# Kernel optimization log

Measured on AMD Instinct MI355X. Metric: run time of the kernel, lower is better.

The kernel has to match this reference:

```python
import jax, jax.numpy as jnp
import numpy as np

FEAT = 128
SCALE = FEAT ** -0.5

def _linear(x, W, b):
    # torch nn.Linear: y = x @ W.T + b, W: [out, in]
    return jnp.einsum('bnd,od->bno', x, W) + b

def setup_inputs() -> dict:
    key = jax.random.key(0)
    ks = jax.random.split(key, 12)
    B, N1, N2 = 2, 4096, 32768
    inp = {
        'sparse_xyz':  jax.random.normal(ks[0], (B, N1, 3),    dtype=jnp.float32),
        'sparse_feat': jax.random.normal(ks[1], (B, N1, FEAT), dtype=jnp.float32),
        'dense_xyz':   jax.random.normal(ks[2], (B, N2, 3),    dtype=jnp.float32),
        'dense_feat':  jax.random.normal(ks[3], (B, N2, FEAT), dtype=jnp.float32),
    }
    s_in = (FEAT + 3) ** -0.5  # torch Linear default init bound ~ 1/sqrt(in)
    s_f = FEAT ** -0.5
    inp['Wq'] = jax.random.uniform(ks[4], (FEAT, FEAT + 3), jnp.float32, -s_in, s_in)
    inp['bq'] = jax.random.uniform(ks[5], (FEAT,), jnp.float32, -s_in, s_in)
    inp['Wk'] = jax.random.uniform(ks[6], (FEAT, FEAT + 3), jnp.float32, -s_in, s_in)
    inp['bk'] = jax.random.uniform(ks[7], (FEAT,), jnp.float32, -s_in, s_in)
    inp['Wv'] = jax.random.uniform(ks[8], (FEAT, FEAT), jnp.float32, -s_f, s_f)
    inp['bv'] = jax.random.uniform(ks[9], (FEAT,), jnp.float32, -s_f, s_f)
    inp['Wo'] = jax.random.uniform(ks[10], (FEAT, FEAT), jnp.float32, -s_f, s_f)
    inp['bo'] = jax.random.uniform(ks[11], (FEAT,), jnp.float32, -s_f, s_f)
    return inp

def reference(sparse_xyz, sparse_feat, dense_xyz, dense_feat,
              Wq, bq, Wk, bk, Wv, bv, Wo, bo):
    # Projections
    Q = _linear(jnp.concatenate([dense_xyz, dense_feat], axis=-1), Wq, bq)   # [B,N2,F]
    K = _linear(jnp.concatenate([sparse_xyz, sparse_feat], axis=-1), Wk, bk) # [B,N1,F]
    V = _linear(sparse_feat, Wv, bv)                                          # [B,N1,F]
    # Attention scores with euclidean distance penalty (torch.cdist, p=2)
    scores = jnp.einsum('bqf,bkf->bqk', Q, K) * SCALE                         # [B,N2,N1]
    sq = (jnp.sum(dense_xyz**2, -1)[:, :, None]
          + jnp.sum(sparse_xyz**2, -1)[:, None, :]
          - 2.0 * jnp.einsum('bqd,bkd->bqk', dense_xyz, sparse_xyz))
    dist = jnp.sqrt(jnp.maximum(sq, 1e-12))
    attn = jax.nn.softmax(scores - 0.5 * dist, axis=-1)                       # [B,N2,N1]
    propagated = jnp.einsum('bqk,bkf->bqf', attn, V)                          # [B,N2,F]
    return _linear(propagated + dense_feat, Wo, bo)
```

## Files before the change

kernel.cpp:

```cpp
#include <hip/hip_runtime.h>
#include <stdint.h>

#define NB 2
#define N1 4096
#define N2 32768
#define DD 128
#define KT 32
#define NTILES (N1 / KT)
static constexpr float SCLE = 0.1275174306f;
static constexpr float CNEG = -0.7213475204444817f;
static constexpr float THR  = 11.5415603f;

typedef float f32x16 __attribute__((ext_vector_type(16)));
typedef __bf16 bf16x8v __attribute__((ext_vector_type(8)));
typedef __bf16 bf16x2v __attribute__((ext_vector_type(2)));
typedef unsigned int u32;
typedef unsigned short u16;

union FragU { uint4 u; bf16x8v b; };

__device__ __forceinline__ u16 f2bf(float f) {
  __bf16 h = (__bf16)f;
  return __builtin_bit_cast(u16, h);
}
__device__ __forceinline__ u32 pk2(float lo, float hi) {
  bf16x2v v; v[0] = (__bf16)lo; v[1] = (__bf16)hi;
  return __builtin_bit_cast(u32, v);
}
__device__ __forceinline__ float bfhi(float f) { return (float)(__bf16)f; }
__device__ __forceinline__ float m3(float a, float b, float c) {
  return fmaxf(fmaxf(a, b), c);
}
__device__ __forceinline__ f32x16 MFMA(uint4 a, uint4 b, const f32x16& c) {
  FragU A, B; A.u = a; B.u = b;
  return __builtin_amdgcn_mfma_f32_32x32x16_bf16(A.b, B.b, c, 0, 0, 0);
}
__device__ __forceinline__ uint4 packhi8(float4 a, float4 b) {
  return make_uint4(pk2(a.x, a.y), pk2(a.z, a.w), pk2(b.x, b.y), pk2(b.z, b.w));
}
__device__ __forceinline__ uint4 packlo8(float4 a, float4 b) {
  return make_uint4(pk2(a.x - bfhi(a.x), a.y - bfhi(a.y)),
                    pk2(a.z - bfhi(a.z), a.w - bfhi(a.w)),
                    pk2(b.x - bfhi(b.x), b.y - bfhi(b.y)),
                    pk2(b.z - bfhi(b.z), b.w - bfhi(b.w)));
}
__device__ __forceinline__ uint4 conv8(float a0, float a1, float a2, float a3,
                                       float a4, float a5, float a6, float a7, int h) {
  u32 A0 = pk2(a0, a1), A1 = pk2(a2, a3);
  u32 B0 = pk2(a4, a5), B1 = pk2(a6, a7);
  u32 A0s = (u32)__shfl_xor((int)A0, 32);
  u32 A1s = (u32)__shfl_xor((int)A1, 32);
  u32 B0s = (u32)__shfl_xor((int)B0, 32);
  u32 B1s = (u32)__shfl_xor((int)B1, 32);
  return h ? make_uint4(B0s, B1s, B0, B1) : make_uint4(A0, A1, A0s, A1s);
}

__global__ __launch_bounds__(256) void prep_kv(
    const float* __restrict__ sxyz, const float* __restrict__ sfeat,
    const float* __restrict__ Wk, const float* __restrict__ bk,
    const float* __restrict__ Wv, const float* __restrict__ bv,
    u16* __restrict__ Kws, u16* __restrict__ VTws, u16* __restrict__ EKws) {
  const int tid = threadIdx.x;
  const int l = tid & 63, w = tid >> 6, h = l >> 5, ln = l & 31;
  const int b = blockIdx.x >> 7;
  const int kb = (blockIdx.x & 127) * 32;
  const int key = kb + ln;
  const size_t frow = (size_t)(b * N1 + key) * DD;

  uint4 xf[8];
#pragma unroll
  for (int s = 0; s < 8; ++s) {
    const float4* fp = (const float4*)(sfeat + frow + s * 16 + h * 8);
    xf[s] = packhi8(fp[0], fp[1]);
  }
  const float* xp = sxyz + (size_t)(b * N1 + key) * 3;
  float sx = xp[0], sy = xp[1], sz = xp[2];
  uint4 x8 = h ? make_uint4(0, 0, 0, 0)
               : make_uint4(pk2(sx, sy), pk2(sz, 0.f), 0u, 0u);

  f32x16 kacc, vacc;
#pragma unroll
  for (int r = 0; r < 16; ++r) {
    int o = (r & 3) + 8 * (r >> 2) + 4 * h + 32 * w;
    kacc[r] = bk[o];
    vacc[r] = bv[o];
  }

  const int outd = ln + 32 * w;
  const float* wkr = Wk + (size_t)outd * 131;
  const float* wvr = Wv + (size_t)outd * DD;
#pragma unroll
  for (int s = 0; s < 8; ++s) {
    const float* p = wkr + 3 + s * 16 + h * 8;
    uint4 wa = make_uint4(pk2(p[0], p[1]), pk2(p[2], p[3]),
                          pk2(p[4], p[5]), pk2(p[6], p[7]));
    kacc = MFMA(wa, xf[s], kacc);
    const float4* q = (const float4*)(wvr + s * 16 + h * 8);
    vacc = MFMA(packhi8(q[0], q[1]), xf[s], vacc);
  }
  {
    uint4 w8 = h ? make_uint4(0, 0, 0, 0)
                 : make_uint4(pk2(wkr[0], wkr[1]), pk2(wkr[2], 0.f), 0u, 0u);
    kacc = MFMA(w8, x8, kacc);
  }

#pragma unroll
  for (int rq = 0; rq < 4; ++rq) {
    uint2 kv;
    kv.x = pk2(kacc[rq * 4 + 0], kacc[rq * 4 + 1]);
    kv.y = pk2(kacc[rq * 4 + 2], kacc[rq * 4 + 3]);
    *(uint2*)&Kws[(size_t)(b * N1 + key) * DD + w * 32 + rq * 8 + h * 4] = kv;
  }
#pragma unroll
  for (int r = 0; r < 16; ++r) {
    int o = (r & 3) + 8 * (r >> 2) + 4 * h + 32 * w;
    VTws[(size_t)(b * DD + o) * N1 + key] = f2bf(vacc[r]);
  }

  if (tid < 32) {
    int k2i = kb + tid;
    const float* xq = sxyz + (size_t)(b * N1 + k2i) * 3;
    float x = xq[0], y = xq[1], z = xq[2];
    float k2 = x * x + y * y + z * z;
    float xh = bfhi(x), xl = x - xh;
    float yh = bfhi(y), yl = y - yh;
    float zh = bfhi(z), zl = z - zh;
    float k2h = bfhi(k2), k2l = k2 - k2h;
    uint4 e0 = make_uint4(pk2(xh, xl), pk2(xh, yh), pk2(yl, yh), pk2(zh, zl));
    uint4 e1 = make_uint4(pk2(zh, k2h), pk2(k2l, 1.f), pk2(1.f, 0.f), 0u);
    uint4* dst = (uint4*)&EKws[(size_t)(b * N1 + k2i) * 16];
    dst[0] = e0;
    dst[1] = e1;
  }
}

__global__ __launch_bounds__(256, 1) void attn_fwd(
    const float* __restrict__ dxyz, const float* __restrict__ dfeat,
    const float* __restrict__ Wq, const float* __restrict__ bq,
    const float* __restrict__ Wo, const float* __restrict__ bo,
    const u16* __restrict__ Kws, const u16* __restrict__ VTws,
    const u16* __restrict__ EKws, float* __restrict__ out) {
  __shared__ __align__(16) u16 sm[8192];

  const int tid = threadIdx.x;
  const int l = tid & 63, w = tid >> 6, h = l >> 5, ln = l & 31;
  const int b = blockIdx.x >> 7;
  const int qb = (blockIdx.x & 127) * 256;
  const int bN1 = b * N1;
  size_t qrow[2];
  qrow[0] = (size_t)(b * N2 + qb + w * 64 + ln);
  qrow[1] = qrow[0] + 32;

  f32x16 zf;
#pragma unroll
  for (int r = 0; r < 16; ++r) zf[r] = 0.f;

  uint4 eq[2];
  float qx[2], qy[2], qz[2];
#pragma unroll
  for (int g = 0; g < 2; ++g) {
    const float* xp = dxyz + qrow[g] * 3;
    float x = xp[0], y = xp[1], z = xp[2];
    float q2 = x * x + y * y + z * z;
    float xh = bfhi(x), xl = x - xh, yh = bfhi(y), yl = y - yh, zh = bfhi(z), zl = z - zh;
    float q2h = bfhi(q2), q2l = q2 - q2h;
    eq[g] = h ? make_uint4(pk2(-2.f * zl, 1.f), pk2(1.f, q2h), pk2(q2l, 0.f), 0u)
              : make_uint4(pk2(-2.f * xh, -2.f * xh), pk2(-2.f * xl, -2.f * yh),
                           pk2(-2.f * yh, -2.f * yl), pk2(-2.f * zh, -2.f * zh));
    qx[g] = x; qy[g] = y; qz[g] = z;
  }

  uint4 qf[2][8];
  {
    uint4 xf[2][8], x8[2];
#pragma unroll
    for (int g = 0; g < 2; ++g) {
#pragma unroll
      for (int s = 0; s < 8; ++s) {
        const float4* fp = (const float4*)(dfeat + qrow[g] * DD + s * 16 + h * 8);
        xf[g][s] = packhi8(fp[0], fp[1]);
      }
      x8[g] = h ? make_uint4(0, 0, 0, 0)
                : make_uint4(pk2(qx[g], qy[g]), pk2(qz[g], 0.f), 0u, 0u);
    }
#pragma unroll
    for (int ot = 0; ot < 4; ++ot) {
      f32x16 qt[2];
#pragma unroll
      for (int r = 0; r < 16; ++r) {
        float bqv = SCLE * bq[(r & 3) + 8 * (r >> 2) + 4 * h + 32 * ot];
        qt[0][r] = bqv; qt[1][r] = bqv;
      }
      const float* wqr = Wq + (size_t)(ln + 32 * ot) * 131;
#pragma unroll
      for (int s = 0; s < 8; ++s) {
        const float* p = wqr + 3 + s * 16 + h * 8;
        uint4 wa = make_uint4(pk2(SCLE * p[0], SCLE * p[1]), pk2(SCLE * p[2], SCLE * p[3]),
                              pk2(SCLE * p[4], SCLE * p[5]), pk2(SCLE * p[6], SCLE * p[7]));
        qt[0] = MFMA(wa, xf[0][s], qt[0]);
        qt[1] = MFMA(wa, xf[1][s], qt[1]);
      }
      uint4 w8 = h ? make_uint4(0, 0, 0, 0)
                   : make_uint4(pk2(SCLE * wqr[0], SCLE * wqr[1]), pk2(SCLE * wqr[2], 0.f), 0u, 0u);
      qt[0] = MFMA(w8, x8[0], qt[0]);
      qt[1] = MFMA(w8, x8[1], qt[1]);
#pragma unroll
      for (int g = 0; g < 2; ++g) {
        qf[g][2 * ot] = conv8(qt[g][0], qt[g][1], qt[g][2], qt[g][3],
                              qt[g][4], qt[g][5], qt[g][6], qt[g][7], h);
        qf[g][2 * ot + 1] = conv8(qt[g][8], qt[g][9], qt[g][10], qt[g][11],
                                  qt[g][12], qt[g][13], qt[g][14], qt[g][15], h);
      }
    }
  }

  f32x16 oacc[2][4];
#pragma unroll
  for (int g = 0; g < 2; ++g)
#pragma unroll
    for (int ft = 0; ft < 4; ++ft)
#pragma unroll
      for (int r = 0; r < 16; ++r) oacc[g][ft][r] = 0.f;
  float m[2] = {-1e30f, -1e30f}, lsum[2] = {0.f, 0.f};

  const int kr = tid >> 4, kd = tid & 15;
  const int vr = tid >> 2, vd = tid & 3;
  const int kswz = (kd ^ (kr & 7)) * 8;
  const int vswz = (vd ^ ((vr >> 1) & 3)) * 8;
  const int vx = (ln >> 1) & 3;
  const u16* Kb = Kws + (size_t)bN1 * DD;
  const u16* Vb = VTws + (size_t)b * DD * N1;
  uint4 k0g, k1g, v0g, v1g;

#define LOADT(kt)                                                            \
  do {                                                                       \
    k0g = *(const uint4*)&Kb[(size_t)((kt) + kr) * DD + kd * 8];             \
    k1g = *(const uint4*)&Kb[(size_t)((kt) + kr + 16) * DD + kd * 8];        \
    v0g = *(const uint4*)&Vb[(size_t)vr * N1 + (kt) + vd * 8];               \
    v1g = *(const uint4*)&Vb[(size_t)(vr + 64) * N1 + (kt) + vd * 8];        \
  } while (0)
#define WRITET()                                                             \
  do {                                                                       \
    *(uint4*)&sm[kr * 128 + kswz] = k0g;                                     \
    *(uint4*)&sm[(kr + 16) * 128 + kswz] = k1g;                              \
    *(uint4*)&sm[4096 + vr * 32 + vswz] = v0g;                               \
    *(uint4*)&sm[4096 + (vr + 64) * 32 + vswz] = v1g;                        \
  } while (0)

  LOADT(0);
  WRITET();
  uint4 ek = *(const uint4*)&EKws[(size_t)(bN1 + ln) * 16 + h * 8];

  for (int t = 0; t < NTILES; ++t) {
    __syncthreads();
    const bool more = (t + 1 < NTILES);
    if (more) LOADT((t + 1) * KT);

    f32x16 sacc[2];
    sacc[0] = MFMA(ek, eq[0], zf);
    sacc[1] = MFMA(ek, eq[1], zf);
#pragma unroll
    for (int g = 0; g < 2; ++g)
#pragma unroll
      for (int r = 0; r < 16; ++r)
        sacc[g][r] = CNEG * __builtin_amdgcn_sqrtf(fmaxf(sacc[g][r], 0.f));

    {
      const int ktn = more ? (t + 1) * KT : 0;
      ek = *(const uint4*)&EKws[(size_t)(bN1 + ktn + ln) * 16 + h * 8];
    }

    __builtin_amdgcn_s_setprio(1);
#pragma unroll
    for (int kk = 0; kk < 8; ++kk) {
      const uint4 ka = *(const uint4*)&sm[ln * 128 + (((2 * kk + h) ^ (ln & 7)) * 8)];
      sacc[0] = MFMA(ka, qf[0][kk], sacc[0]);
      sacc[1] = MFMA(ka, qf[1][kk], sacc[1]);
    }
    __builtin_amdgcn_s_setprio(0);

    uint4 pf[2][2];
#pragma unroll
    for (int g = 0; g < 2; ++g) {
      float a0 = m3(sacc[g][0], sacc[g][1], sacc[g][2]);
      float a1 = m3(sacc[g][3], sacc[g][4], sacc[g][5]);
      float a2 = m3(sacc[g][6], sacc[g][7], sacc[g][8]);
      float a3 = m3(sacc[g][9], sacc[g][10], sacc[g][11]);
      float a4 = m3(sacc[g][12], sacc[g][13], sacc[g][14]);
      float tmax = fmaxf(m3(m3(a0, a1, a2), a3, a4), sacc[g][15]);
      tmax = fmaxf(tmax, __shfl_xor(tmax, 32));
      if (!__all(tmax <= m[g] + THR)) {
        float nm = fmaxf(m[g], tmax);
        float f = __builtin_amdgcn_exp2f(m[g] - nm);
        lsum[g] *= f;
#pragma unroll
        for (int ft = 0; ft < 4; ++ft)
#pragma unroll
          for (int r = 0; r < 16; ++r) oacc[g][ft][r] *= f;
        m[g] = nm;
      }
#pragma unroll
      for (int r = 0; r < 16; ++r)
        sacc[g][r] = __builtin_amdgcn_exp2f(sacc[g][r] - m[g]);
      {
        float s0 = sacc[g][0] + sacc[g][1],   s1 = sacc[g][2] + sacc[g][3];
        float s2 = sacc[g][4] + sacc[g][5],   s3 = sacc[g][6] + sacc[g][7];
        float s4 = sacc[g][8] + sacc[g][9],   s5 = sacc[g][10] + sacc[g][11];
        float s6 = sacc[g][12] + sacc[g][13], s7 = sacc[g][14] + sacc[g][15];
        lsum[g] += (s0 + s1) + (s2 + s3) + ((s4 + s5) + (s6 + s7));
      }
      pf[g][0] = conv8(sacc[g][0], sacc[g][1], sacc[g][2], sacc[g][3],
                       sacc[g][4], sacc[g][5], sacc[g][6], sacc[g][7], h);
      pf[g][1] = conv8(sacc[g][8], sacc[g][9], sacc[g][10], sacc[g][11],
                       sacc[g][12], sacc[g][13], sacc[g][14], sacc[g][15], h);
    }

    __builtin_amdgcn_s_setprio(1);
#pragma unroll
    for (int ft = 0; ft < 4; ++ft) {
      const int rr = 32 * ft + ln;
      const uint4 va0 = *(const uint4*)&sm[4096 + rr * 32 + ((h ^ vx) * 8)];
      oacc[0][ft] = MFMA(va0, pf[0][0], oacc[0][ft]);
      oacc[1][ft] = MFMA(va0, pf[1][0], oacc[1][ft]);
      const uint4 va1 = *(const uint4*)&sm[4096 + rr * 32 + (((2 + h) ^ vx) * 8)];
      oacc[0][ft] = MFMA(va1, pf[0][1], oacc[0][ft]);
      oacc[1][ft] = MFMA(va1, pf[1][1], oacc[1][ft]);
    }
    __builtin_amdgcn_s_setprio(0);

    __syncthreads();
    if (more) WRITET();
  }
#undef LOADT
#undef WRITET

#pragma unroll
  for (int g = 0; g < 2; ++g) {
    lsum[g] += __shfl_xor(lsum[g], 32);
    const float inv = 1.f / lsum[g];
#pragma unroll
    for (int ft = 0; ft < 4; ++ft)
#pragma unroll
      for (int r = 0; r < 16; ++r) oacc[g][ft][r] *= inv;
  }

  f32x16 oc[2][4];
#pragma unroll
  for (int g = 0; g < 2; ++g)
#pragma unroll
    for (int ot = 0; ot < 4; ++ot)
#pragma unroll
      for (int r = 0; r < 16; ++r)
        oc[g][ot][r] = bo[(r & 3) + 8 * (r >> 2) + 4 * h + 32 * ot];

#pragma unroll
  for (int s = 0; s < 8; ++s) {
    uint4 pb[2], fh[2], fl[2];
#pragma unroll
    for (int g = 0; g < 2; ++g) {
      const f32x16& c = oacc[g][s >> 1];
      const int br = (s & 1) * 8;
      pb[g] = conv8(c[br + 0], c[br + 1], c[br + 2], c[br + 3],
                    c[br + 4], c[br + 5], c[br + 6], c[br + 7], h);
      const float4* fp = (const float4*)(dfeat + qrow[g] * DD + s * 16 + h * 8);
      const float4 fa = fp[0], fb = fp[1];
      fh[g] = packhi8(fa, fb);
      fl[g] = packlo8(fa, fb);
    }
#pragma unroll
    for (int ot = 0; ot < 4; ++ot) {
      const float4* wp = (const float4*)(Wo + (size_t)(ln + 32 * ot) * DD + s * 16 + h * 8);
      const float4 wa = wp[0], wb = wp[1];
      const uint4 wh = packhi8(wa, wb);
      const uint4 wl = packlo8(wa, wb);
#pragma unroll
      for (int g = 0; g < 2; ++g) {
        oc[g][ot] = MFMA(wh, pb[g], oc[g][ot]);
        oc[g][ot] = MFMA(wh, fh[g], oc[g][ot]);
        oc[g][ot] = MFMA(wh, fl[g], oc[g][ot]);
        oc[g][ot] = MFMA(wl, fh[g], oc[g][ot]);
      }
    }
  }

#pragma unroll
  for (int g = 0; g < 2; ++g) {
    float* orow = out + qrow[g] * DD;
#pragma unroll
    for (int ot = 0; ot < 4; ++ot)
#pragma unroll
      for (int rq = 0; rq < 4; ++rq)
        *(float4*)&orow[ot * 32 + rq * 8 + h * 4] =
            make_float4(oc[g][ot][rq * 4 + 0], oc[g][ot][rq * 4 + 1],
                        oc[g][ot][rq * 4 + 2], oc[g][ot][rq * 4 + 3]);
  }
}

extern "C" void kernel_launch(void* const* d_in, const int* in_sizes, int n_in,
                              void* d_out, int out_size, void* d_ws, size_t ws_size,
                              hipStream_t stream) {
  const float* sxyz = (const float*)d_in[0];
  const float* sfeat = (const float*)d_in[1];
  const float* dxyz = (const float*)d_in[2];
  const float* dfeat = (const float*)d_in[3];
  const float* Wq = (const float*)d_in[4];
  const float* bq = (const float*)d_in[5];
  const float* Wk = (const float*)d_in[6];
  const float* bk = (const float*)d_in[7];
  const float* Wv = (const float*)d_in[8];
  const float* bv = (const float*)d_in[9];
  const float* Wo = (const float*)d_in[10];
  const float* bo = (const float*)d_in[11];

  u16* Kws = (u16*)d_ws;
  u16* VTws = Kws + (size_t)NB * N1 * DD;
  u16* EKws = VTws + (size_t)NB * DD * N1;

  prep_kv<<<dim3(NB * 128), dim3(256), 0, stream>>>(sxyz, sfeat, Wk, bk, Wv, bv,
                                                    Kws, VTws, EKws);
  attn_fwd<<<dim3(NB * 128), dim3(256), 0, stream>>>(dxyz, dfeat, Wq, bq, Wo, bo,
                                                     Kws, VTws, EKws, (float*)d_out);
}
```

Before: 383.1 us.

## Double-buffer K and triple-buffer V in LDS, deferring the PV MFMA one tile

Shared memory grows so K tiles are double-buffered and V tiles triple-buffered. Global loads are issued two tiles ahead, and each iteration needs only one barrier instead of two. The P·V MFMA for tile t-1 is moved to the start of iteration t, ahead of the QK MFMA for tile t, so the softmax work can overlap with tensor-core work. The cost is more LDS (40 KB) and extra registers to keep the pf fragments live across iterations.

```diff
diff --git a/kernel.cpp b/kernel.cpp
--- a/kernel.cpp
+++ b/kernel.cpp
@@ -140,7 +140,7 @@
     const float* __restrict__ Wo, const float* __restrict__ bo,
     const u16* __restrict__ Kws, const u16* __restrict__ VTws,
     const u16* __restrict__ EKws, float* __restrict__ out) {
-  __shared__ __align__(16) u16 sm[8192];
+  __shared__ __align__(16) u16 sm[20480];
 
   const int tid = threadIdx.x;
   const int l = tid & 63, w = tid >> 6, h = l >> 5, ln = l & 31;
@@ -239,22 +239,25 @@
     v0g = *(const uint4*)&Vb[(size_t)vr * N1 + (kt) + vd * 8];               \
     v1g = *(const uint4*)&Vb[(size_t)(vr + 64) * N1 + (kt) + vd * 8];        \
   } while (0)
-#define WRITET()                                                             \
+#define WRITET(kb_, vb_)                                                     \
   do {                                                                       \
-    *(uint4*)&sm[kr * 128 + kswz] = k0g;                                     \
-    *(uint4*)&sm[(kr + 16) * 128 + kswz] = k1g;                              \
-    *(uint4*)&sm[4096 + vr * 32 + vswz] = v0g;                               \
-    *(uint4*)&sm[4096 + (vr + 64) * 32 + vswz] = v1g;                        \
+    *(uint4*)&sm[(kb_) + kr * 128 + kswz] = k0g;                             \
+    *(uint4*)&sm[(kb_) + (kr + 16) * 128 + kswz] = k1g;                      \
+    *(uint4*)&sm[(vb_) + vr * 32 + vswz] = v0g;                              \
+    *(uint4*)&sm[(vb_) + (vr + 64) * 32 + vswz] = v1g;                       \
   } while (0)
 
   LOADT(0);
-  WRITET();
+  WRITET(0, 8192);
+  LOADT(KT);
   uint4 ek = *(const uint4*)&EKws[(size_t)(bN1 + ln) * 16 + h * 8];
+  __syncthreads();
+
+  uint4 pf[2][2];
+  int vr3 = 2, vw3 = 1;
 
   for (int t = 0; t < NTILES; ++t) {
-    __syncthreads();
-    const bool more = (t + 1 < NTILES);
-    if (more) LOADT((t + 1) * KT);
+    if (t + 1 < NTILES) WRITET(((t + 1) & 1) * 4096, 8192 + vw3 * 4096);
 
     f32x16 sacc[2];
     sacc[0] = MFMA(ek, eq[0], zf);
@@ -265,21 +268,38 @@
       for (int r = 0; r < 16; ++r)
         sacc[g][r] = CNEG * __builtin_amdgcn_sqrtf(fmaxf(sacc[g][r], 0.f));
 
+    if (t + 2 < NTILES) LOADT((t + 2) * KT);
     {
-      const int ktn = more ? (t + 1) * KT : 0;
+      const int ktn = (t + 1 < NTILES) ? (t + 1) * KT : 0;
       ek = *(const uint4*)&EKws[(size_t)(bN1 + ktn + ln) * 16 + h * 8];
     }
 
     __builtin_amdgcn_s_setprio(1);
-#pragma unroll
-    for (int kk = 0; kk < 8; ++kk) {
-      const uint4 ka = *(const uint4*)&sm[ln * 128 + (((2 * kk + h) ^ (ln & 7)) * 8)];
-      sacc[0] = MFMA(ka, qf[0][kk], sacc[0]);
-      sacc[1] = MFMA(ka, qf[1][kk], sacc[1]);
+    if (t > 0) {
+      const int vbr = 8192 + vr3 * 4096;
+#pragma unroll
+      for (int ft = 0; ft < 4; ++ft) {
+        const int rr = 32 * ft + ln;
+        const uint4 va0 = *(const uint4*)&sm[vbr + rr * 32 + ((h ^ vx) * 8)];
+        oacc[0][ft] = MFMA(va0, pf[0][0], oacc[0][ft]);
+        oacc[1][ft] = MFMA(va0, pf[1][0], oacc[1][ft]);
+        const uint4 va1 = *(const uint4*)&sm[vbr + rr * 32 + (((2 + h) ^ vx) * 8)];
+        oacc[0][ft] = MFMA(va1, pf[0][1], oacc[0][ft]);
+        oacc[1][ft] = MFMA(va1, pf[1][1], oacc[1][ft]);
+      }
+    }
+
+    {
+      const int kbr = (t & 1) * 4096;
+#pragma unroll
+      for (int kk = 0; kk < 8; ++kk) {
+        const uint4 ka = *(const uint4*)&sm[kbr + ln * 128 + (((2 * kk + h) ^ (ln & 7)) * 8)];
+        sacc[0] = MFMA(ka, qf[0][kk], sacc[0]);
+        sacc[1] = MFMA(ka, qf[1][kk], sacc[1]);
+      }
     }
     __builtin_amdgcn_s_setprio(0);
 
-    uint4 pf[2][2];
 #pragma unroll
     for (int g = 0; g < 2; ++g) {
       float a0 = m3(sacc[g][0], sacc[g][1], sacc[g][2]);
@@ -315,21 +335,23 @@
                        sacc[g][12], sacc[g][13], sacc[g][14], sacc[g][15], h);
     }
 
-    __builtin_amdgcn_s_setprio(1);
+    __syncthreads();
+    vr3 = (vr3 == 2) ? 0 : vr3 + 1;
+    vw3 = (vw3 == 2) ? 0 : vw3 + 1;
+  }
+
+  {
+    const int vbr = 8192 + vr3 * 4096;
 #pragma unroll
     for (int ft = 0; ft < 4; ++ft) {
       const int rr = 32 * ft + ln;
-      const uint4 va0 = *(const uint4*)&sm[4096 + rr * 32 + ((h ^ vx) * 8)];
+      const uint4 va0 = *(const uint4*)&sm[vbr + rr * 32 + ((h ^ vx) * 8)];
       oacc[0][ft] = MFMA(va0, pf[0][0], oacc[0][ft]);
       oacc[1][ft] = MFMA(va0, pf[1][0], oacc[1][ft]);
-      const uint4 va1 = *(const uint4*)&sm[4096 + rr * 32 + (((2 + h) ^ vx) * 8)];
+      const uint4 va1 = *(const uint4*)&sm[vbr + rr * 32 + (((2 + h) ^ vx) * 8)];
       oacc[0][ft] = MFMA(va1, pf[0][1], oacc[0][ft]);
       oacc[1][ft] = MFMA(va1, pf[1][1], oacc[1][ft]);
     }
-    __builtin_amdgcn_s_setprio(0);
-
-    __syncthreads();
-    if (more) WRITET();
   }
 #undef LOADT
 #undef WRITET
```

Result: faster. 356.2 us (-7.0%).

## Pre-swizzle K/V into MFMA fragment layout and stream per-wave from global

Applied to the files above, without the earlier changes.

The prep kernel now writes K and V tiles directly in MFMA operand fragment order, with V transposed through shared memory. Each wave can then load its operands straight from global or L2 with coalesced 16-byte loads. The attention kernel becomes one wave per block (1024 blocks), dropping the shared-memory staging and all __syncthreads. It adds register double-buffering and software pipelining, so the PV product of the previous tile overlaps the load and QK of the next. The cost is higher register pressure and redundant global/L2 traffic, since every wave now reads all of K and V without sharing through LDS.

```diff
diff --git a/kernel.cpp b/kernel.cpp
--- a/kernel.cpp
+++ b/kernel.cpp
@@ -59,11 +59,13 @@
     const float* __restrict__ sxyz, const float* __restrict__ sfeat,
     const float* __restrict__ Wk, const float* __restrict__ bk,
     const float* __restrict__ Wv, const float* __restrict__ bv,
-    u16* __restrict__ Kws, u16* __restrict__ VTws, u16* __restrict__ EKws) {
+    uint4* __restrict__ Kf, uint4* __restrict__ Vf, u16* __restrict__ EKws) {
+  __shared__ __align__(16) u16 sv[128 * 32];
   const int tid = threadIdx.x;
   const int l = tid & 63, w = tid >> 6, h = l >> 5, ln = l & 31;
   const int b = blockIdx.x >> 7;
-  const int kb = (blockIdx.x & 127) * 32;
+  const int tile = blockIdx.x & 127;
+  const int kb = tile * 32;
   const int key = kb + ln;
   const size_t frow = (size_t)(b * N1 + key) * DD;
 
@@ -104,17 +106,25 @@
     kacc = MFMA(w8, x8, kacc);
   }
 
-#pragma unroll
-  for (int rq = 0; rq < 4; ++rq) {
-    uint2 kv;
-    kv.x = pk2(kacc[rq * 4 + 0], kacc[rq * 4 + 1]);
-    kv.y = pk2(kacc[rq * 4 + 2], kacc[rq * 4 + 3]);
-    *(uint2*)&Kws[(size_t)(b * N1 + key) * DD + w * 32 + rq * 8 + h * 4] = kv;
-  }
+  const size_t fbase = ((size_t)(b * NTILES + tile)) * 8;
+  {
+    uint4 kf0 = conv8(kacc[0], kacc[1], kacc[2], kacc[3],
+                      kacc[4], kacc[5], kacc[6], kacc[7], h);
+    uint4 kf1 = conv8(kacc[8], kacc[9], kacc[10], kacc[11],
+                      kacc[12], kacc[13], kacc[14], kacc[15], h);
+    Kf[(fbase + 2 * w + 0) * 64 + l] = kf0;
+    Kf[(fbase + 2 * w + 1) * 64 + l] = kf1;
+  }
+
 #pragma unroll
   for (int r = 0; r < 16; ++r) {
     int o = (r & 3) + 8 * (r >> 2) + 4 * h + 32 * w;
-    VTws[(size_t)(b * DD + o) * N1 + key] = f2bf(vacc[r]);
+    sv[o * 32 + ln] = f2bf(vacc[r]);
+  }
+#pragma unroll
+  for (int s = 0; s < 2; ++s) {
+    uint4 va = *(const uint4*)&sv[(32 * w + ln) * 32 + 16 * s + 8 * h];
+    Vf[(fbase + 2 * w + s) * 64 + l] = va;
   }
 
   if (tid < 32) {
@@ -134,21 +144,18 @@
   }
 }
 
-__global__ __launch_bounds__(256, 1) void attn_fwd(
+__global__ __launch_bounds__(64, 1) void attn_fwd(
     const float* __restrict__ dxyz, const float* __restrict__ dfeat,
     const float* __restrict__ Wq, const float* __restrict__ bq,
     const float* __restrict__ Wo, const float* __restrict__ bo,
-    const u16* __restrict__ Kws, const u16* __restrict__ VTws,
+    const uint4* __restrict__ Kf, const uint4* __restrict__ Vf,
     const u16* __restrict__ EKws, float* __restrict__ out) {
-  __shared__ __align__(16) u16 sm[8192];
-
-  const int tid = threadIdx.x;
-  const int l = tid & 63, w = tid >> 6, h = l >> 5, ln = l & 31;
-  const int b = blockIdx.x >> 7;
-  const int qb = (blockIdx.x & 127) * 256;
+  const int l = threadIdx.x, ln = l & 31, h = l >> 5;
+  const int b = blockIdx.x >> 9;
+  const int qb = (blockIdx.x & 511) * 64;
   const int bN1 = b * N1;
   size_t qrow[2];
-  qrow[0] = (size_t)(b * N2 + qb + w * 64 + ln);
+  qrow[0] = (size_t)(b * N2 + qb + ln);
   qrow[1] = qrow[0] + 32;
 
   f32x16 zf;
@@ -223,116 +230,98 @@
       for (int r = 0; r < 16; ++r) oacc[g][ft][r] = 0.f;
   float m[2] = {-1e30f, -1e30f}, lsum[2] = {0.f, 0.f};
 
-  const int kr = tid >> 4, kd = tid & 15;
-  const int vr = tid >> 2, vd = tid & 3;
-  const int kswz = (kd ^ (kr & 7)) * 8;
-  const int vswz = (vd ^ ((vr >> 1) & 3)) * 8;
-  const int vx = (ln >> 1) & 3;
-  const u16* Kb = Kws + (size_t)bN1 * DD;
-  const u16* Vb = VTws + (size_t)b * DD * N1;
-  uint4 k0g, k1g, v0g, v1g;
-
-#define LOADT(kt)                                                            \
-  do {                                                                       \
-    k0g = *(const uint4*)&Kb[(size_t)((kt) + kr) * DD + kd * 8];             \
-    k1g = *(const uint4*)&Kb[(size_t)((kt) + kr + 16) * DD + kd * 8];        \
-    v0g = *(const uint4*)&Vb[(size_t)vr * N1 + (kt) + vd * 8];               \
-    v1g = *(const uint4*)&Vb[(size_t)(vr + 64) * N1 + (kt) + vd * 8];        \
+  const uint4* Kfb = Kf + (size_t)b * NTILES * 8 * 64;
+  const uint4* Vfb = Vf + (size_t)b * NTILES * 8 * 64;
+  const uint4* EK4 = (const uint4*)EKws;
+
+  uint4 kbuf[2][8], vbuf[2][8], ekb[2];
+  uint4 pf[2][2];
+
+#define LOADF(BUF, t_)                                                        \
+  do {                                                                        \
+    _Pragma("unroll")                                                         \
+    for (int f_ = 0; f_ < 8; ++f_) {                                          \
+      kbuf[BUF][f_] = Kfb[((size_t)(t_) * 8 + f_) * 64 + l];                  \
+      vbuf[BUF][f_] = Vfb[((size_t)(t_) * 8 + f_) * 64 + l];                  \
+    }                                                                         \
+    ekb[BUF] = EK4[((size_t)(bN1 + (t_) * KT + ln)) * 2 + h];                 \
   } while (0)
-#define WRITET()                                                             \
-  do {                                                                       \
-    *(uint4*)&sm[kr * 128 + kswz] = k0g;                                     \
-    *(uint4*)&sm[(kr + 16) * 128 + kswz] = k1g;                              \
-    *(uint4*)&sm[4096 + vr * 32 + vswz] = v0g;                               \
-    *(uint4*)&sm[4096 + (vr + 64) * 32 + vswz] = v1g;                        \
-  } while (0)
-
-  LOADT(0);
-  WRITET();
-  uint4 ek = *(const uint4*)&EKws[(size_t)(bN1 + ln) * 16 + h * 8];
-
-  for (int t = 0; t < NTILES; ++t) {
-    __syncthreads();
-    const bool more = (t + 1 < NTILES);
-    if (more) LOADT((t + 1) * KT);
-
-    f32x16 sacc[2];
-    sacc[0] = MFMA(ek, eq[0], zf);
-    sacc[1] = MFMA(ek, eq[1], zf);
-#pragma unroll
-    for (int g = 0; g < 2; ++g)
-#pragma unroll
-      for (int r = 0; r < 16; ++r)
-        sacc[g][r] = CNEG * __builtin_amdgcn_sqrtf(fmaxf(sacc[g][r], 0.f));
-
-    {
-      const int ktn = more ? (t + 1) * KT : 0;
-      ek = *(const uint4*)&EKws[(size_t)(bN1 + ktn + ln) * 16 + h * 8];
-    }
-
-    __builtin_amdgcn_s_setprio(1);
-#pragma unroll
-    for (int kk = 0; kk < 8; ++kk) {
-      const uint4 ka = *(const uint4*)&sm[ln * 128 + (((2 * kk + h) ^ (ln & 7)) * 8)];
-      sacc[0] = MFMA(ka, qf[0][kk], sacc[0]);
-      sacc[1] = MFMA(ka, qf[1][kk], sacc[1]);
-    }
-    __builtin_amdgcn_s_setprio(0);
-
-    uint4 pf[2][2];
-#pragma unroll
-    for (int g = 0; g < 2; ++g) {
-      float a0 = m3(sacc[g][0], sacc[g][1], sacc[g][2]);
-      float a1 = m3(sacc[g][3], sacc[g][4], sacc[g][5]);
-      float a2 = m3(sacc[g][6], sacc[g][7], sacc[g][8]);
-      float a3 = m3(sacc[g][9], sacc[g][10], sacc[g][11]);
-      float a4 = m3(sacc[g][12], sacc[g][13], sacc[g][14]);
-      float tmax = fmaxf(m3(m3(a0, a1, a2), a3, a4), sacc[g][15]);
-      tmax = fmaxf(tmax, __shfl_xor(tmax, 32));
-      if (!__all(tmax <= m[g] + THR)) {
-        float nm = fmaxf(m[g], tmax);
-        float f = __builtin_amdgcn_exp2f(m[g] - nm);
-        lsum[g] *= f;
-#pragma unroll
-        for (int ft = 0; ft < 4; ++ft)
-#pragma unroll
-          for (int r = 0; r < 16; ++r) oacc[g][ft][r] *= f;
-        m[g] = nm;
-      }
-#pragma unroll
-      for (int r = 0; r < 16; ++r)
-        sacc[g][r] = __builtin_amdgcn_exp2f(sacc[g][r] - m[g]);
-      {
-        float s0 = sacc[g][0] + sacc[g][1],   s1 = sacc[g][2] + sacc[g][3];
-        float s2 = sacc[g][4] + sacc[g][5],   s3 = sacc[g][6] + sacc[g][7];
-        float s4 = sacc[g][8] + sacc[g][9],   s5 = sacc[g][10] + sacc[g][11];
-        float s6 = sacc[g][12] + sacc[g][13], s7 = sacc[g][14] + sacc[g][15];
-        lsum[g] += (s0 + s1) + (s2 + s3) + ((s4 + s5) + (s6 + s7));
-      }
-      pf[g][0] = conv8(sacc[g][0], sacc[g][1], sacc[g][2], sacc[g][3],
-                       sacc[g][4], sacc[g][5], sacc[g][6], sacc[g][7], h);
-      pf[g][1] = conv8(sacc[g][8], sacc[g][9], sacc[g][10], sacc[g][11],
-                       sacc[g][12], sacc[g][13], sacc[g][14], sacc[g][15], h);
-    }
-
-    __builtin_amdgcn_s_setprio(1);
-#pragma unroll
-    for (int ft = 0; ft < 4; ++ft) {
-      const int rr = 32 * ft + ln;
-      const uint4 va0 = *(const uint4*)&sm[4096 + rr * 32 + ((h ^ vx) * 8)];
-      oacc[0][ft] = MFMA(va0, pf[0][0], oacc[0][ft]);
-      oacc[1][ft] = MFMA(va0, pf[1][0], oacc[1][ft]);
-      const uint4 va1 = *(const uint4*)&sm[4096 + rr * 32 + (((2 + h) ^ vx) * 8)];
-      oacc[0][ft] = MFMA(va1, pf[0][1], oacc[0][ft]);
-      oacc[1][ft] = MFMA(va1, pf[1][1], oacc[1][ft]);
-    }
-    __builtin_amdgcn_s_setprio(0);
-
-    __syncthreads();
-    if (more) WRITET();
-  }
-#undef LOADT
-#undef WRITET
+
+#define ITER(t_, CUR, NXT)                                                    \
+  {                                                                           \
+    f32x16 sacc[2];                                                           \
+    sacc[0] = MFMA(ekb[CUR], eq[0], zf);                                      \
+    sacc[1] = MFMA(ekb[CUR], eq[1], zf);                                      \
+    _Pragma("unroll")                                                         \
+    for (int g = 0; g < 2; ++g)                                               \
+      _Pragma("unroll")                                                       \
+      for (int r = 0; r < 16; ++r)                                            \
+        sacc[g][r] = CNEG * __builtin_amdgcn_sqrtf(fmaxf(sacc[g][r], 0.f));   \
+    if ((t_) > 0) {             \
+      _Pragma("unroll")                                                       \
+      for (int ft = 0; ft < 4; ++ft) {                                        \
+        oacc[0][ft] = MFMA(vbuf[NXT][2 * ft], pf[0][0], oacc[0][ft]);         \
+        oacc[1][ft] = MFMA(vbuf[NXT][2 * ft], pf[1][0], oacc[1][ft]);         \
+        oacc[0][ft] = MFMA(vbuf[NXT][2 * ft + 1], pf[0][1], oacc[0][ft]);     \
+        oacc[1][ft] = MFMA(vbuf[NXT][2 * ft + 1], pf[1][1], oacc[1][ft]);     \
+      }                                                                       \
+    }                                                                         \
+    if ((t_) + 1 < NTILES) LOADF(NXT, (t_) + 1);                              \
+    _Pragma("unroll")                               \
+    for (int kk = 0; kk < 8; ++kk) {                                          \
+      sacc[0] = MFMA(kbuf[CUR][kk], qf[0][kk], sacc[0]);                      \
+      sacc[1] = MFMA(kbuf[CUR][kk], qf[1][kk], sacc[1]);                      \
+    }                                                                         \
+    _Pragma("unroll")                 \
+    for (int g = 0; g < 2; ++g) {                                             \
+      float a0 = m3(sacc[g][0], sacc[g][1], sacc[g][2]);                      \
+      float a1 = m3(sacc[g][3], sacc[g][4], sacc[g][5]);                      \
+      float a2 = m3(sacc[g][6], sacc[g][7], sacc[g][8]);                      \
+      float a3 = m3(sacc[g][9], sacc[g][10], sacc[g][11]);                    \
+      float a4 = m3(sacc[g][12], sacc[g][13], sacc[g][14]);                   \
+      float tmax = fmaxf(m3(m3(a0, a1, a2), a3, a4), sacc[g][15]);            \
+      tmax = fmaxf(tmax, __shfl_xor(tmax, 32));                               \
+      if (!__all(tmax <= m[g] + THR)) {                                       \
+        float nm = fmaxf(m[g], tmax);                                         \
+        float fr = __builtin_amdgcn_exp2f(m[g] - nm);                         \
+        lsum[g] *= fr;                                                        \
+        _Pragma("unroll")                                                     \
+        for (int ft = 0; ft < 4; ++ft)                                        \
+          _Pragma("unroll")                                                   \
+          for (int r = 0; r < 16; ++r) oacc[g][ft][r] *= fr;                  \
+        m[g] = nm;                                                            \
+      }                                                                       \
+      _Pragma("unroll")                                                       \
+      for (int r = 0; r < 16; ++r)                                            \
+        sacc[g][r] = __builtin_amdgcn_exp2f(sacc[g][r] - m[g]);               \
+      {                                                                       \
+        float s0 = sacc[g][0] + sacc[g][1],   s1 = sacc[g][2] + sacc[g][3];   \
+        float s2 = sacc[g][4] + sacc[g][5],   s3 = sacc[g][6] + sacc[g][7];   \
+        float s4 = sacc[g][8] + sacc[g][9],   s5 = sacc[g][10] + sacc[g][11]; \
+        float s6 = sacc[g][12] + sacc[g][13], s7 = sacc[g][14] + sacc[g][15]; \
+        lsum[g] += (s0 + s1) + (s2 + s3) + ((s4 + s5) + (s6 + s7));           \
+      }                                                                       \
+      pf[g][0] = conv8(sacc[g][0], sacc[g][1], sacc[g][2], sacc[g][3],        \
+                       sacc[g][4], sacc[g][5], sacc[g][6], sacc[g][7], h);    \
+      pf[g][1] = conv8(sacc[g][8], sacc[g][9], sacc[g][10], sacc[g][11],      \
+                       sacc[g][12], sacc[g][13], sacc[g][14], sacc[g][15], h);\
+    }                                                                         \
+  }
+
+  LOADF(0, 0);
+  for (int t = 0; t < NTILES; t += 2) {
+    ITER(t, 0, 1);
+    ITER(t + 1, 1, 0);
+  }
+#pragma unroll
+  for (int ft = 0; ft < 4; ++ft) {
+    oacc[0][ft] = MFMA(vbuf[1][2 * ft], pf[0][0], oacc[0][ft]);
+    oacc[1][ft] = MFMA(vbuf[1][2 * ft], pf[1][0], oacc[1][ft]);
+    oacc[0][ft] = MFMA(vbuf[1][2 * ft + 1], pf[0][1], oacc[0][ft]);
+    oacc[1][ft] = MFMA(vbuf[1][2 * ft + 1], pf[1][1], oacc[1][ft]);
+  }
+#undef LOADF
+#undef ITER
 
 #pragma unroll
   for (int g = 0; g < 2; ++g) {
@@ -412,12 +401,12 @@
   const float* Wo = (const float*)d_in[10];
   const float* bo = (const float*)d_in[11];
 
-  u16* Kws = (u16*)d_ws;
-  u16* VTws = Kws + (size_t)NB * N1 * DD;
-  u16* EKws = VTws + (size_t)NB * DD * N1;
+  uint4* Kf = (uint4*)d_ws;
+  uint4* Vf = Kf + (size_t)NB * NTILES * 8 * 64;
+  u16* EKws = (u16*)(Vf + (size_t)NB * NTILES * 8 * 64);
 
   prep_kv<<<dim3(NB * 128), dim3(256), 0, stream>>>(sxyz, sfeat, Wk, bk, Wv, bv,
-                                                    Kws, VTws, EKws);
-  attn_fwd<<<dim3(NB * 128), dim3(256), 0, stream>>>(dxyz, dfeat, Wq, bq, Wo, bo,
-                                                     Kws, VTws, EKws, (float*)d_out);
-}
+                                                    Kf, Vf, EKws);
+  attn_fwd<<<dim3(NB * 512), dim3(64), 0, stream>>>(dxyz, dfeat, Wq, bq, Wo, bo,
+                                                    Kf, Vf, EKws, (float*)d_out);
+}
```

Result: slower. 504.1 us (+31.6%).
